# Kernel tuning notes

Hardware: AMD Instinct MI355X
Metric: run time of the kernel (lower is better)

## Reference

```python
import jax, jax.numpy as jnp
import numpy as np

K = 27          # kernel_size^3
N_IN = 150000   # active input sites
N_OUT = 150000  # active output sites
C_IN = 64
C_OUT = 64
R = 50000       # rules per kernel offset (equal counts -> vectorized grouped GEMM)


def setup_inputs() -> dict:
    key = jax.random.key(0)
    k1, k2, k3, k4 = jax.random.split(key, 4)
    # kaiming_normal_ fan_out, relu: std = sqrt(2 / fan_out) with fan_out = C_OUT
    w_std = float(np.sqrt(2.0 / C_OUT))
    return {
        "x_data": jax.random.normal(k1, (N_IN, C_IN), dtype=jnp.float32),
        "weights": jax.random.normal(k2, (K, C_IN, C_OUT), dtype=jnp.float32) * w_std,
        "bias": jnp.zeros((C_OUT,), dtype=jnp.float32),
        "in_idx": jax.random.randint(k3, (K * R,), 0, N_IN, dtype=jnp.int32),
        "out_idx": jax.random.randint(k4, (K * R,), 0, N_OUT, dtype=jnp.int32),
    }


def reference(x_data, weights, bias, in_idx, out_idx):
    # Rulebook sparse 3D conv: per-offset gather -> GEMM -> scatter-add.
    gathered = x_data[in_idx].reshape(K, R, C_IN)           # [K, R, Cin]
    vals = jnp.einsum('krc,kco->kro', gathered, weights)    # [K, R, Cout]
    out = jnp.zeros((N_OUT, C_OUT), dtype=x_data.dtype)
    out = out.at[out_idx].add(vals.reshape(K * R, C_OUT))   # atomic scatter-add
    return out + bias[None, :]
```

## Files before the change

### kernel.cpp

```cpp
#include <hip/hip_runtime.h>
#include <hip/hip_bf16.h>


typedef __bf16 bf16x8_t __attribute__((ext_vector_type(8)));
typedef __bf16 bf16x4_t __attribute__((ext_vector_type(4)));
typedef __bf16 bf16x2_t __attribute__((ext_vector_type(2)));
typedef float f32x4_t __attribute__((ext_vector_type(4)));

#define KOFF 27
#define RULES 50000
#define KR (KOFF * RULES)
#define CIN 64
#define COUT 64
#define NIN 150000
#define NOUT 150000

#define BR1 128
#define BPK1 ((RULES + BR1 - 1) / BR1)
#define BRF 256
#define BPKF ((RULES + BRF - 1) / BRF)

#define OFF_OFF 0ull
#define OFF_BSUM 600064ull
#define OFF_RANK 600832ull
#define OFF_XB 6000896ull
#define OFF_VALS 25200896ull
#define WS_FULL (25200896ull + 172800000ull)

__device__ __forceinline__ void gload_lds16(const void* g, void* l) {
  __builtin_amdgcn_global_load_lds(
      (const __attribute__((address_space(1))) unsigned int*)g,
      (__attribute__((address_space(3))) unsigned int*)l, 16, 0, 0);
}

__global__ __launch_bounds__(256) void k_cvt_zero(const float* __restrict__ x,
                                                  __bf16* __restrict__ xb,
                                                  int* __restrict__ cnt) {
  const int i = blockIdx.x * 256 + threadIdx.x;
  if (i < NIN * CIN / 8) {
    const float4 f0 = reinterpret_cast<const float4*>(x)[i * 2];
    const float4 f1 = reinterpret_cast<const float4*>(x)[i * 2 + 1];
    bf16x8_t v;
    v[0] = (__bf16)f0.x; v[1] = (__bf16)f0.y; v[2] = (__bf16)f0.z; v[3] = (__bf16)f0.w;
    v[4] = (__bf16)f1.x; v[5] = (__bf16)f1.y; v[6] = (__bf16)f1.z; v[7] = (__bf16)f1.w;
    reinterpret_cast<bf16x8_t*>(xb)[i] = v;
  }
  if (i <= NOUT) cnt[i] = 0;
}

__global__ __launch_bounds__(256) void k_count(const int* __restrict__ out_idx,
                                               int* __restrict__ cnt,
                                               int* __restrict__ rankl) {
  const int i = blockIdx.x * 256 + threadIdx.x;
  if (i < KR / 4) {
    const int4 v = reinterpret_cast<const int4*>(out_idx)[i];
    int4 r;
    r.x = atomicAdd(&cnt[v.x], 1);
    r.y = atomicAdd(&cnt[v.y], 1);
    r.z = atomicAdd(&cnt[v.z], 1);
    r.w = atomicAdd(&cnt[v.w], 1);
    reinterpret_cast<int4*>(rankl)[i] = r;
  }
}

__global__ __launch_bounds__(1024) void k_scan1(int* __restrict__ off,
                                                int* __restrict__ bsum) {
  __shared__ int s[1024];
  const int t = threadIdx.x;
  const int i = blockIdx.x * 1024 + t;
  const int v = (i < NOUT) ? off[i] : 0;
  s[t] = v;
  __syncthreads();
#pragma unroll
  for (int d = 1; d < 1024; d <<= 1) {
    const int u = (t >= d) ? s[t - d] : 0;
    __syncthreads();
    s[t] += u;
    __syncthreads();
  }
  if (i < NOUT) off[i] = s[t] - v;
  if (t == 1023) bsum[blockIdx.x] = s[1023];
}

__global__ __launch_bounds__(256) void k_scan2(int* __restrict__ bsum, int nb) {
  __shared__ int s[256];
  const int t = threadIdx.x;
  const int v = (t < nb) ? bsum[t] : 0;
  s[t] = v;
  __syncthreads();
#pragma unroll
  for (int d = 1; d < 256; d <<= 1) {
    const int u = (t >= d) ? s[t - d] : 0;
    __syncthreads();
    s[t] += u;
    __syncthreads();
  }
  if (t < nb) bsum[t] = s[t] - v;
}

__global__ __launch_bounds__(256) void k_scan3(int* __restrict__ off,
                                               const int* __restrict__ bsum) {
  const int i = blockIdx.x * 256 + threadIdx.x;
  if (i < NOUT) off[i] += bsum[i >> 10];
  if (i == 0) off[NOUT] = KR;
}

__global__ __launch_bounds__(256) void pass1_bf16(
    const __bf16* __restrict__ xb, const float* __restrict__ w,
    const int* __restrict__ in_idx, const int* __restrict__ out_idx,
    const int* __restrict__ off_arr, const int* __restrict__ rankl,
    __bf16* __restrict__ vals) {
  __shared__ char lds[BR1 * 128 + 64 * 128];
  char* const Abase = lds;
  char* const Bbase = lds + BR1 * 128;

  const int bid = blockIdx.x;
  const int k = bid / BPK1;
  const int rblk = bid - k * BPK1;
  const int rule0 = rblk * BR1;
  const int t = threadIdx.x;
  const int wid = t >> 6;
  const int lane = t & 63;

  {
    const int rowInWave = lane >> 3;
    const int srcChunk = (lane & 7) ^ rowInWave;
    const int* idxBase = in_idx + (size_t)k * RULES;
#pragma unroll
    for (int it = 0; it < 4; ++it) {
      const int rbase = it * 32 + wid * 8;
      int rule = rule0 + rbase + rowInWave;
      if (rule > RULES - 1) rule = RULES - 1;
      const int src = idxBase[rule];
      const __bf16* gp = xb + ((size_t)src << 6) + (srcChunk << 3);
      gload_lds16(gp, Abase + rbase * 128 + lane * 16);
    }
  }

  {
    const int c = t >> 2;
    const int o0 = (t & 3) * 16;
    const float* wp = w + ((size_t)k * CIN + c) * COUT + o0;
#pragma unroll
    for (int j4 = 0; j4 < 4; ++j4) {
      const float4 f = *reinterpret_cast<const float4*>(wp + j4 * 4);
#pragma unroll
      for (int e = 0; e < 4; ++e) {
        const int o = o0 + j4 * 4 + e;
        const float val = (e == 0) ? f.x : (e == 1) ? f.y : (e == 2) ? f.z : f.w;
        const int addr = o * 128 + ((c * 2) ^ ((o & 7) << 4));
        *reinterpret_cast<__bf16*>(Bbase + addr) = (__bf16)val;
      }
    }
  }

  __syncthreads();

  const int rA = lane & 15;
  const int g = lane >> 4;

  bf16x8_t af[2][2];
  bf16x8_t bfr[4][2];
#pragma unroll
  for (int m = 0; m < 2; ++m)
#pragma unroll
    for (int kk = 0; kk < 2; ++kk) {
      const int r = wid * 32 + m * 16 + rA;
      const int colByte = (kk * 64 + g * 16) ^ ((r & 7) << 4);
      af[m][kk] = *reinterpret_cast<const bf16x8_t*>(Abase + r * 128 + colByte);
    }
#pragma unroll
  for (int n = 0; n < 4; ++n)
#pragma unroll
    for (int kk = 0; kk < 2; ++kk) {
      const int o = n * 16 + rA;
      const int colByte = (kk * 64 + g * 16) ^ ((o & 7) << 4);
      bfr[n][kk] = *reinterpret_cast<const bf16x8_t*>(Bbase + o * 128 + colByte);
    }

  __syncthreads();

  f32x4_t acc[2][4];
#pragma unroll
  for (int m = 0; m < 2; ++m)
#pragma unroll
    for (int n = 0; n < 4; ++n)
#pragma unroll
      for (int e = 0; e < 4; ++e) acc[m][n][e] = 0.0f;

#pragma unroll
  for (int kk = 0; kk < 2; ++kk)
#pragma unroll
    for (int m = 0; m < 2; ++m)
#pragma unroll
      for (int n = 0; n < 4; ++n)
        acc[m][n] = __builtin_amdgcn_mfma_f32_16x16x32_bf16(
            af[m][kk], bfr[n][kk], acc[m][n], 0, 0, 0);

  const bool evenLane = (rA & 1) == 0;
#pragma unroll
  for (int m = 0; m < 2; ++m) {
#pragma unroll
    for (int j = 0; j < 4; ++j) {
      const int rr = wid * 32 + m * 16 + g * 4 + j;
      float mine[4], other[4];
#pragma unroll
      for (int n = 0; n < 4; ++n) {
        mine[n] = acc[m][n][j];
        other[n] = __shfl_xor(mine[n], 1, 64);
      }
      const int swz = (rr & 7) << 4;
      if (evenLane) {
#pragma unroll
        for (int n = 0; n < 2; ++n) {
          bf16x2_t p; p[0] = (__bf16)mine[n]; p[1] = (__bf16)other[n];
          const int col = n * 16 + rA;
          *reinterpret_cast<bf16x2_t*>(Abase + rr * 128 + ((col * 2) ^ swz)) = p;
        }
      } else {
#pragma unroll
        for (int n = 2; n < 4; ++n) {
          bf16x2_t p; p[0] = (__bf16)other[n]; p[1] = (__bf16)mine[n];
          const int col = n * 16 + rA - 1;
          *reinterpret_cast<bf16x2_t*>(Abase + rr * 128 + ((col * 2) ^ swz)) = p;
        }
      }
    }
  }

  __syncthreads();

  {
    const int chunk = t & 7;
    const int r0 = t >> 3;
#pragma unroll
    for (int pass = 0; pass < 4; ++pass) {
      const int r = r0 + pass * 32;
      const int rule = rule0 + r;
      if (rule < RULES) {
        const size_t gi = (size_t)k * RULES + rule;
        const int dst = off_arr[out_idx[gi]] + rankl[gi];
        const bf16x8_t v = *reinterpret_cast<const bf16x8_t*>(
            Abase + r * 128 + ((chunk * 16) ^ ((r & 7) << 4)));
        *reinterpret_cast<bf16x8_t*>(vals + (size_t)dst * COUT + chunk * 8) = v;
      }
    }
  }
}

__global__ __launch_bounds__(256) void pass2_kernel(
    const __bf16* __restrict__ vals, const int* __restrict__ off,
    const float* __restrict__ bias, float* __restrict__ out) {
  const int t = threadIdx.x;
  const int rloc = t >> 4;
  const int l16 = t & 15;
  const int row = blockIdx.x * 16 + rloc;
  if (row >= NOUT) return;

  const float4 b = reinterpret_cast<const float4*>(bias)[l16];
  float a0 = b.x, a1 = b.y, a2 = b.z, a3 = b.w;

  const int r0 = off[row];
  const int r1 = off[row + 1];
  const __bf16* vp = vals + (size_t)r0 * COUT + l16 * 4;
  for (int j = r0; j < r1; ++j, vp += COUT) {
    const bf16x4_t v = *reinterpret_cast<const bf16x4_t*>(vp);
    a0 += (float)v[0];
    a1 += (float)v[1];
    a2 += (float)v[2];
    a3 += (float)v[3];
  }
  reinterpret_cast<float4*>(out + (size_t)row * COUT)[l16] =
      make_float4(a0, a1, a2, a3);
}

__global__ __launch_bounds__(256) void init_out_kernel(
    const float* __restrict__ bias, float* __restrict__ out, int total4) {
  const int i = blockIdx.x * blockDim.x + threadIdx.x;
  if (i < total4) {
    const float4 v = reinterpret_cast<const float4*>(bias)[i & 15];
    reinterpret_cast<float4*>(out)[i] = v;
  }
}

__global__ __launch_bounds__(256) void spconv_atomic_kernel(
    const float* __restrict__ x, const float* __restrict__ w,
    const int* __restrict__ in_idx, const int* __restrict__ out_idx,
    float* __restrict__ out) {
  __shared__ char lds[256 * 128 + 64 * 128];
  char* const Abase = lds;
  char* const Bbase = lds + 256 * 128;

  const int bid = blockIdx.x;
  const int k = bid / BPKF;
  const int rblk = bid - k * BPKF;
  const int rule0 = rblk * BRF;
  const int t = threadIdx.x;

  {
    const int chunk = t & 7;
    const int r0 = t >> 3;
#pragma unroll
    for (int pass = 0; pass < 8; ++pass) {
      const int r = r0 + pass * 32;
      const int rule = rule0 + r;
      bf16x8_t v;
      if (rule < RULES) {
        const int src = in_idx[(size_t)k * RULES + rule];
        const float* p = x + (size_t)src * CIN + chunk * 8;
        const float4 f0 = *reinterpret_cast<const float4*>(p);
        const float4 f1 = *reinterpret_cast<const float4*>(p + 4);
        v[0] = (__bf16)f0.x; v[1] = (__bf16)f0.y;
        v[2] = (__bf16)f0.z; v[3] = (__bf16)f0.w;
        v[4] = (__bf16)f1.x; v[5] = (__bf16)f1.y;
        v[6] = (__bf16)f1.z; v[7] = (__bf16)f1.w;
      } else {
#pragma unroll
        for (int e = 0; e < 8; ++e) v[e] = (__bf16)0.0f;
      }
      const int colByte = (chunk * 16) ^ ((r & 7) << 4);
      *reinterpret_cast<bf16x8_t*>(Abase + r * 128 + colByte) = v;
    }
  }
  {
    const int c = t >> 2;
    const int o0 = (t & 3) * 16;
    const float* wp = w + ((size_t)k * CIN + c) * COUT + o0;
#pragma unroll
    for (int j4 = 0; j4 < 4; ++j4) {
      const float4 f = *reinterpret_cast<const float4*>(wp + j4 * 4);
#pragma unroll
      for (int e = 0; e < 4; ++e) {
        const int o = o0 + j4 * 4 + e;
        const float val = (e == 0) ? f.x : (e == 1) ? f.y : (e == 2) ? f.z : f.w;
        const int addr = o * 128 + ((c * 2) ^ ((o & 7) << 4));
        *reinterpret_cast<__bf16*>(Bbase + addr) = (__bf16)val;
      }
    }
  }
  __syncthreads();

  const int wid = t >> 6;
  const int l = t & 63;
  const int rA = l & 15;
  const int g = l >> 4;

  bf16x8_t af[4][2];
  bf16x8_t bfr[4][2];
#pragma unroll
  for (int m = 0; m < 4; ++m)
#pragma unroll
    for (int kk = 0; kk < 2; ++kk) {
      const int r = wid * 64 + m * 16 + rA;
      const int colByte = (kk * 64 + g * 16) ^ ((r & 7) << 4);
      af[m][kk] = *reinterpret_cast<const bf16x8_t*>(Abase + r * 128 + colByte);
    }
#pragma unroll
  for (int n = 0; n < 4; ++n)
#pragma unroll
    for (int kk = 0; kk < 2; ++kk) {
      const int o = n * 16 + rA;
      const int colByte = (kk * 64 + g * 16) ^ ((o & 7) << 4);
      bfr[n][kk] = *reinterpret_cast<const bf16x8_t*>(Bbase + o * 128 + colByte);
    }

  f32x4_t acc[4][4];
#pragma unroll
  for (int m = 0; m < 4; ++m)
#pragma unroll
    for (int n = 0; n < 4; ++n)
#pragma unroll
      for (int e = 0; e < 4; ++e) acc[m][n][e] = 0.0f;

#pragma unroll
  for (int kk = 0; kk < 2; ++kk)
#pragma unroll
    for (int m = 0; m < 4; ++m)
#pragma unroll
      for (int n = 0; n < 4; ++n)
        acc[m][n] = __builtin_amdgcn_mfma_f32_16x16x32_bf16(
            af[m][kk], bfr[n][kk], acc[m][n], 0, 0, 0);

#pragma unroll
  for (int m = 0; m < 4; ++m)
#pragma unroll
    for (int j = 0; j < 4; ++j) {
      const int rr = wid * 64 + m * 16 + g * 4 + j;
      const int rule = rule0 + rr;
      if (rule < RULES) {
        const int orow = out_idx[(size_t)k * RULES + rule];
        float* op = out + (size_t)orow * COUT + rA;
#pragma unroll
        for (int n = 0; n < 4; ++n) atomicAdd(op + n * 16, acc[m][n][j]);
      }
    }
}

extern "C" void kernel_launch(void* const* d_in, const int* in_sizes, int n_in,
                              void* d_out, int out_size, void* d_ws, size_t ws_size,
                              hipStream_t stream) {
  const float* x = (const float*)d_in[0];
  const float* w = (const float*)d_in[1];
  const float* bias = (const float*)d_in[2];
  const int* in_idx = (const int*)d_in[3];
  const int* out_idx = (const int*)d_in[4];
  float* out = (float*)d_out;

  if (ws_size >= WS_FULL) {
    char* ws = (char*)d_ws;
    int* off = (int*)(ws + OFF_OFF);
    int* bsum = (int*)(ws + OFF_BSUM);
    int* rankl = (int*)(ws + OFF_RANK);
    __bf16* xb = (__bf16*)(ws + OFF_XB);
    __bf16* vals = (__bf16*)(ws + OFF_VALS);

    const int nb1 = (NOUT + 1023) / 1024;
    k_cvt_zero<<<(NIN * CIN / 8 + 255) / 256, 256, 0, stream>>>(x, xb, off);
    k_count<<<(KR / 4 + 255) / 256, 256, 0, stream>>>(out_idx, off, rankl);
    k_scan1<<<nb1, 1024, 0, stream>>>(off, bsum);
    k_scan2<<<1, 256, 0, stream>>>(bsum, nb1);
    k_scan3<<<(NOUT + 255) / 256, 256, 0, stream>>>(off, bsum);
    pass1_bf16<<<KOFF * BPK1, 256, 0, stream>>>(xb, w, in_idx, out_idx, off,
                                                rankl, vals);
    pass2_kernel<<<(NOUT + 15) / 16, 256, 0, stream>>>(vals, off, bias, out);
  } else {
    const int total4 = NOUT * COUT / 4;
    init_out_kernel<<<(total4 + 255) / 256, 256, 0, stream>>>(bias, out, total4);
    spconv_atomic_kernel<<<KOFF * BPKF, 256, 0, stream>>>(x, w, in_idx, out_idx, out);
  }
}
```

Baseline: 274.1 us.

## Fuse scan kernels, prefetch scatter destinations, stage pass2 rows via LDS

```diff
diff --git a/kernel.cpp b/kernel.cpp
--- a/kernel.cpp
+++ b/kernel.cpp
@@ -17,6 +17,8 @@
 
 #define BR1 128
 #define BPK1 ((RULES + BR1 - 1) / BR1)
+#define P2R 16
+#define P2CH 256
 #define BRF 256
 #define BPKF ((RULES + BRF - 1) / BRF)
 
@@ -82,7 +84,9 @@
   if (t == 1023) bsum[blockIdx.x] = s[1023];
 }
 
-__global__ __launch_bounds__(256) void k_scan2(int* __restrict__ bsum, int nb) {
+__global__ __launch_bounds__(256) void k_scan3(int* __restrict__ off,
+                                               const int* __restrict__ bsum,
+                                               int nb) {
   __shared__ int s[256];
   const int t = threadIdx.x;
   const int v = (t < nb) ? bsum[t] : 0;
@@ -95,13 +99,11 @@
     s[t] += u;
     __syncthreads();
   }
-  if (t < nb) bsum[t] = s[t] - v;
-}
-
-__global__ __launch_bounds__(256) void k_scan3(int* __restrict__ off,
-                                               const int* __restrict__ bsum) {
-  const int i = blockIdx.x * 256 + threadIdx.x;
-  if (i < NOUT) off[i] += bsum[i >> 10];
+  const int i = blockIdx.x * 256 + t;
+  if (i < NOUT) {
+    const int b = i >> 10;
+    off[i] += s[b] - bsum[b];
+  }
   if (i == 0) off[NOUT] = KR;
 }
 
@@ -111,6 +113,7 @@
     const int* __restrict__ off_arr, const int* __restrict__ rankl,
     __bf16* __restrict__ vals) {
   __shared__ char lds[BR1 * 128 + 64 * 128];
+  __shared__ int lds_dst[BR1];
   char* const Abase = lds;
   char* const Bbase = lds + BR1 * 128;
 
@@ -137,6 +140,14 @@
     }
   }
 
+  if (t < BR1) {
+    const int rule = rule0 + t;
+    if (rule < RULES) {
+      const size_t gi = (size_t)k * RULES + rule;
+      lds_dst[t] = off_arr[out_idx[gi]] + rankl[gi];
+    }
+  }
+
   {
     const int c = t >> 2;
     const int o0 = (t & 3) * 16;
@@ -238,8 +249,7 @@
       const int r = r0 + pass * 32;
       const int rule = rule0 + r;
       if (rule < RULES) {
-        const size_t gi = (size_t)k * RULES + rule;
-        const int dst = off_arr[out_idx[gi]] + rankl[gi];
+        const int dst = lds_dst[r];
         const bf16x8_t v = *reinterpret_cast<const bf16x8_t*>(
             Abase + r * 128 + ((chunk * 16) ^ ((r & 7) << 4)));
         *reinterpret_cast<bf16x8_t*>(vals + (size_t)dst * COUT + chunk * 8) = v;
@@ -251,27 +261,53 @@
 __global__ __launch_bounds__(256) void pass2_kernel(
     const __bf16* __restrict__ vals, const int* __restrict__ off,
     const float* __restrict__ bias, float* __restrict__ out) {
+  __shared__ __bf16 buf[P2CH * COUT];
+  __shared__ int soff[P2R + 1];
+
   const int t = threadIdx.x;
+  const int row0 = blockIdx.x * P2R;
+
+  if (t <= P2R) {
+    int r = row0 + t;
+    if (r > NOUT) r = NOUT;
+    soff[t] = off[r];
+  }
+  __syncthreads();
+
+  const int S = soff[0];
+  const int E = soff[P2R];
   const int rloc = t >> 4;
   const int l16 = t & 15;
-  const int row = blockIdx.x * 16 + rloc;
-  if (row >= NOUT) return;
+  const int r0 = soff[rloc];
+  const int r1 = soff[rloc + 1];
 
   const float4 b = reinterpret_cast<const float4*>(bias)[l16];
   float a0 = b.x, a1 = b.y, a2 = b.z, a3 = b.w;
 
-  const int r0 = off[row];
-  const int r1 = off[row + 1];
-  const __bf16* vp = vals + (size_t)r0 * COUT + l16 * 4;
-  for (int j = r0; j < r1; ++j, vp += COUT) {
-    const bf16x4_t v = *reinterpret_cast<const bf16x4_t*>(vp);
-    a0 += (float)v[0];
-    a1 += (float)v[1];
-    a2 += (float)v[2];
-    a3 += (float)v[3];
-  }
-  reinterpret_cast<float4*>(out + (size_t)row * COUT)[l16] =
-      make_float4(a0, a1, a2, a3);
+  for (int base = S; base < E; base += P2CH) {
+    const int n = min(P2CH, E - base);
+    for (int u = t; u < n * 8; u += 256)
+      gload_lds16(vals + ((size_t)base << 6) + (size_t)u * 8,
+                  (char*)buf + (size_t)u * 16);
+    __syncthreads();
+
+    const int js = (r0 > base) ? r0 : base;
+    const int je = (r1 < base + n) ? r1 : (base + n);
+    const char* bp = (const char*)buf + (size_t)(js - base) * 128 + l16 * 8;
+    for (int j = js; j < je; ++j, bp += 128) {
+      const bf16x4_t v = *reinterpret_cast<const bf16x4_t*>(bp);
+      a0 += (float)v[0];
+      a1 += (float)v[1];
+      a2 += (float)v[2];
+      a3 += (float)v[3];
+    }
+    __syncthreads();
+  }
+
+  const int row = row0 + rloc;
+  if (row < NOUT)
+    reinterpret_cast<float4*>(out + (size_t)row * COUT)[l16] =
+        make_float4(a0, a1, a2, a3);
 }
 
 __global__ __launch_bounds__(256) void init_out_kernel(
@@ -418,11 +454,10 @@
     k_cvt_zero<<<(NIN * CIN / 8 + 255) / 256, 256, 0, stream>>>(x, xb, off);
     k_count<<<(KR / 4 + 255) / 256, 256, 0, stream>>>(out_idx, off, rankl);
     k_scan1<<<nb1, 1024, 0, stream>>>(off, bsum);
-    k_scan2<<<1, 256, 0, stream>>>(bsum, nb1);
-    k_scan3<<<(NOUT + 255) / 256, 256, 0, stream>>>(off, bsum);
+    k_scan3<<<(NOUT + 255) / 256, 256, 0, stream>>>(off, bsum, nb1);
     pass1_bf16<<<KOFF * BPK1, 256, 0, stream>>>(xb, w, in_idx, out_idx, off,
                                                 rankl, vals);
-    pass2_kernel<<<(NOUT + 15) / 16, 256, 0, stream>>>(vals, off, bias, out);
+    pass2_kernel<<<(NOUT + P2R - 1) / P2R, 256, 0, stream>>>(vals, off, bias, out);
   } else {
     const int total4 = NOUT * COUT / 4;
     init_out_kernel<<<(total4 + 255) / 256, 256, 0, stream>>>(bias, out, total4);
```

New measurement: 261.9 us. 1.05x faster.
